# Performance work log

Measured on AMD Instinct MI355X. Metric: run time of the kernel, lower is better.

Reference implementation:

```python
import jax, jax.numpy as jnp
import numpy as np

B, S, D = 4, 4096, 128

def setup_inputs() -> dict:
    key = jax.random.key(0)
    kx, kq, kk, kv = jax.random.split(key, 4)
    x = jax.random.normal(kx, (B, S, D), dtype=jnp.float32)
    Wq = jax.random.normal(kq, (D, D), dtype=jnp.float32) * (1.0 / np.sqrt(D))
    Wk = jax.random.normal(kk, (D, D), dtype=jnp.float32) * (1.0 / np.sqrt(D))
    Wv = jax.random.normal(kv, (D, D), dtype=jnp.float32) * (1.0 / np.sqrt(D))
    return {"x": x, "Wq": Wq, "Wk": Wk, "Wv": Wv}

def reference(x, Wq, Wk, Wv):
    b, s, d = x.shape
    # nn.Linear(bias=False): y = x @ W.T
    q = jnp.einsum('bsd,ed->bse', x, Wq)
    k = jnp.einsum('bsd,ed->bse', x, Wk)
    v = jnp.einsum('bsd,ed->bse', x, Wv)
    scores = jnp.einsum('bqd,bkd->bqk', q, k) / jnp.sqrt(jnp.float32(d))
    causal = jnp.tril(jnp.ones((s, s), dtype=bool))  # [s,s]
    scores = jnp.where(causal, scores, jnp.float32(-jnp.inf))
    weights = jax.nn.softmax(scores.astype(jnp.float32), axis=-1)
    out = jnp.einsum('bqk,bkd->bqd', weights, v)
    return out  # dropout is identity in eval / p=0
```

## Files before the change

kernel.cpp:

```cpp
#include <hip/hip_runtime.h>
#include <hip/hip_bf16.h>
#include <math.h>

typedef __attribute__((ext_vector_type(8))) short short8;
typedef __attribute__((ext_vector_type(4))) float f32x4;
typedef __attribute__((ext_vector_type(4))) float float4v;
typedef __attribute__((ext_vector_type(4))) unsigned short ushort4v;

typedef __attribute__((address_space(1))) const unsigned int GAS;
typedef __attribute__((address_space(3))) unsigned int LAS;

#define B_ 4
#define S_ 4096
#define D_ 128

#define CHUNKS_PER_BATCH 288
#define NSLOT (B_ * CHUNKS_PER_BATCH)

#define LDS_K 0
#define LDS_V 16384
#define LDS_P 49152
#define LDS_TOTAL 57344

__device__ __forceinline__ unsigned short f2bf(float f) {
    union { float f; unsigned u; } v; v.f = f;
    unsigned r = v.u + 0x7FFFu + ((v.u >> 16) & 1u);
    return (unsigned short)(r >> 16);
}
__device__ __forceinline__ float bf2f(unsigned short h) {
    union { unsigned u; float f; } v; v.u = ((unsigned)h) << 16;
    return v.f;
}

__global__ void wconv_kernel(const float* __restrict__ Wq,
                             const float* __restrict__ Wk,
                             const float* __restrict__ Wv,
                             unsigned short* __restrict__ Wb) {
    int i = blockIdx.x * 256 + threadIdx.x;
    if (i >= 3 * 16384) return;
    const float* s = (i < 16384) ? Wq : (i < 32768 ? Wk : Wv);
    Wb[i] = f2bf(s[i & 16383]);
}

__global__ __launch_bounds__(256) void qkv_kernel(const float* __restrict__ X,
                                                  const unsigned short* __restrict__ Wb,
                                                  unsigned short* __restrict__ Qb,
                                                  unsigned short* __restrict__ Kb,
                                                  unsigned short* __restrict__ Vt) {
    const int tid = threadIdx.x;
    const int lane = tid & 63, w = tid >> 6;
    const int l16 = lane & 15, g = lane >> 4;
    const int r0 = blockIdx.x * 64;
    const int grp = blockIdx.y;

    const int row = r0 + w * 16 + l16;
    const float* xr = X + (long)row * 128;
    float4v x0[4], x1[4];
    #pragma unroll
    for (int kb = 0; kb < 4; ++kb) {
        x0[kb] = *reinterpret_cast<const float4v*>(xr + kb * 32 + g * 8);
        x1[kb] = *reinterpret_cast<const float4v*>(xr + kb * 32 + g * 8 + 4);
    }
    short8 a[4];
    #pragma unroll
    for (int kb = 0; kb < 4; ++kb) {
        short8 t;
        t[0] = f2bf(x0[kb][0]); t[1] = f2bf(x0[kb][1]);
        t[2] = f2bf(x0[kb][2]); t[3] = f2bf(x0[kb][3]);
        t[4] = f2bf(x1[kb][0]); t[5] = f2bf(x1[kb][1]);
        t[6] = f2bf(x1[kb][2]); t[7] = f2bf(x1[kb][3]);
        a[kb] = t;
    }

    #pragma unroll
    for (int ct = 0; ct < 8; ++ct) {
        const int e = ct * 16 + l16;
        const int c = grp * 128 + e;
        f32x4 acc = {0.f, 0.f, 0.f, 0.f};
        #pragma unroll
        for (int kb = 0; kb < 4; ++kb) {
            short8 bf = *reinterpret_cast<const short8*>(Wb + (long)c * 128 + kb * 32 + g * 8);
            acc = __builtin_amdgcn_mfma_f32_16x16x32_bf16(a[kb], bf, acc, 0, 0, 0);
        }
        const int row0 = r0 + w * 16 + g * 4;
        if (grp == 0) {
            #pragma unroll
            for (int r = 0; r < 4; ++r) Qb[(long)(row0 + r) * 128 + e] = f2bf(acc[r]);
        } else if (grp == 1) {
            #pragma unroll
            for (int r = 0; r < 4; ++r) Kb[(long)(row0 + r) * 128 + e] = f2bf(acc[r]);
        } else {
            const int bb = row0 >> 12, ss = row0 & 4095;
            ushort4v p;
            p[0] = f2bf(acc[0]); p[1] = f2bf(acc[1]); p[2] = f2bf(acc[2]); p[3] = f2bf(acc[3]);
            *reinterpret_cast<ushort4v*>(&Vt[((long)bb * 128 + e) * 4096 + ss]) = p;
        }
    }
}

__global__ __launch_bounds__(256) void attn_kernel(const unsigned short* __restrict__ Qb,
                                                   const unsigned short* __restrict__ Kb,
                                                   const unsigned short* __restrict__ Vt,
                                                   unsigned short* __restrict__ Opart,
                                                   float* __restrict__ Mpart,
                                                   float* __restrict__ Lpart) {
    __shared__ __align__(16) unsigned char lds[LDS_TOTAL];

    const int tid = threadIdx.x;
    const int lane = tid & 63, w = tid >> 6;
    const int l16 = lane & 15, g = lane >> 4;

    const int bidx = (int)blockIdx.x;
    const int b = bidx / CHUNKS_PER_BATCH;
    const int rr = bidx - b * CHUNKS_PER_BATCH;
    int gg = 0;
    while (4 * (gg + 1) * (gg + 2) <= rr) ++gg;
    const int j = rr - 4 * gg * (gg + 1);
    const int qt = 8 * gg + j / (gg + 1);
    const int c = j % (gg + 1);
    const int slot = bidx;

    const unsigned short* Qbase = Qb + (long)b * S_ * D_;
    const unsigned char* Kb_b = (const unsigned char*)(Kb + (long)b * S_ * D_);
    const unsigned char* Vb_b = (const unsigned char*)(Vt + (long)b * D_ * S_);

    const int qrow_f = qt * 64 + w * 16 + l16;
    short8 qf[4];
    #pragma unroll
    for (int kb = 0; kb < 4; ++kb)
        qf[kb] = *reinterpret_cast<const short8*>(Qbase + (long)qrow_f * 128 + kb * 32 + g * 8);

    int koff[4], voff[4];
    #pragma unroll
    for (int i = 0; i < 4; ++i) {
        int ch = w * 4 + i;
        int krow = ch * 4 + g;
        koff[i] = krow * 256 + ((l16 * 16) ^ ((krow & 7) << 4));
        int vrow = ch * 8 + (lane >> 3);
        voff[i] = vrow * 8192 + (((lane & 7) * 16) ^ ((vrow & 7) << 4));
    }

    f32x4 o[8];
    #pragma unroll
    for (int dt = 0; dt < 8; ++dt) o[dt] = (f32x4){0.f, 0.f, 0.f, 0.f};
    float m[4], lsum[4];
    int myrow[4];
    #pragma unroll
    for (int r = 0; r < 4; ++r) {
        m[r] = -INFINITY; lsum[r] = 0.f;
        myrow[r] = qt * 64 + w * 16 + g * 4 + r;
    }

    const float scale = 0.08838834764831845f;
    const int kt0 = c * 8;
    const int ktend = min(kt0 + 7, qt);

    #pragma unroll
    for (int i = 0; i < 4; ++i) {
        int ch = w * 4 + i;
        __builtin_amdgcn_global_load_lds((GAS*)(Kb_b + (long)kt0 * 16384 + koff[i]),
                                         (LAS*)(lds + LDS_K + ch * 1024), 16, 0, 0);
        __builtin_amdgcn_global_load_lds((GAS*)(Vb_b + (long)kt0 * 128 + voff[i]),
                                         (LAS*)(lds + LDS_V + (kt0 & 1) * 16384 + ch * 1024), 16, 0, 0);
    }
    __syncthreads();

    for (int kt = kt0; kt <= ktend; ++kt) {
        const int buf = kt & 1;
        const bool more = (kt < ktend);

        f32x4 s[4];
        #pragma unroll
        for (int ct = 0; ct < 4; ++ct) {
            s[ct] = (f32x4){0.f, 0.f, 0.f, 0.f};
            const int kvl = ct * 16 + l16;
            #pragma unroll
            for (int kb = 0; kb < 4; ++kb) {
                int byt = (kvl * 256 + kb * 64 + g * 16) ^ ((kvl & 7) << 4);
                short8 kf = *reinterpret_cast<const short8*>(lds + byt);
                s[ct] = __builtin_amdgcn_mfma_f32_16x16x32_bf16(qf[kb], kf, s[ct], 0, 0, 0);
            }
        }

        __syncthreads();

        if (more) {
            #pragma unroll
            for (int i = 0; i < 4; ++i) {
                int ch = w * 4 + i;
                __builtin_amdgcn_global_load_lds((GAS*)(Kb_b + (long)(kt + 1) * 16384 + koff[i]),
                                                 (LAS*)(lds + LDS_K + ch * 1024), 16, 0, 0);
                __builtin_amdgcn_global_load_lds((GAS*)(Vb_b + (long)(kt + 1) * 128 + voff[i]),
                                                 (LAS*)(lds + LDS_V + (buf ^ 1) * 16384 + ch * 1024), 16, 0, 0);
            }
        }

        const bool diag = (kt == qt);
        float rmax[4] = {-1e30f, -1e30f, -1e30f, -1e30f};
        #pragma unroll
        for (int ct = 0; ct < 4; ++ct) {
            #pragma unroll
            for (int r = 0; r < 4; ++r) {
                float sv = s[ct][r] * scale;
                if (diag && (kt * 64 + ct * 16 + l16 > myrow[r])) sv = -1e30f;
                s[ct][r] = sv;
                rmax[r] = fmaxf(rmax[r], sv);
            }
        }
        #pragma unroll
        for (int off = 1; off < 16; off <<= 1) {
            #pragma unroll
            for (int r = 0; r < 4; ++r) rmax[r] = fmaxf(rmax[r], __shfl_xor(rmax[r], off, 64));
        }
        float al[4], rsum[4];
        #pragma unroll
        for (int r = 0; r < 4; ++r) {
            float mn = fmaxf(m[r], rmax[r]);
            al[r] = __expf(m[r] - mn);
            m[r] = mn;
            rsum[r] = 0.f;
        }
        #pragma unroll
        for (int ct = 0; ct < 4; ++ct) {
            #pragma unroll
            for (int r = 0; r < 4; ++r) {
                float p = __expf(s[ct][r] - m[r]);
                s[ct][r] = p;
                rsum[r] += p;
            }
        }
        #pragma unroll
        for (int off = 1; off < 16; off <<= 1) {
            #pragma unroll
            for (int r = 0; r < 4; ++r) rsum[r] += __shfl_xor(rsum[r], off, 64);
        }
        #pragma unroll
        for (int r = 0; r < 4; ++r) lsum[r] = lsum[r] * al[r] + rsum[r];
        #pragma unroll
        for (int dt = 0; dt < 8; ++dt) {
            #pragma unroll
            for (int r = 0; r < 4; ++r) o[dt][r] *= al[r];
        }

        unsigned char* Pw = lds + LDS_P + w * 2048;
        #pragma unroll
        for (int ct = 0; ct < 4; ++ct) {
            #pragma unroll
            for (int r = 0; r < 4; ++r) {
                int pr = g * 4 + r, pc = ct * 16 + l16;
                int byt = (pr * 128 + pc * 2) ^ ((pr & 7) << 4);
                *reinterpret_cast<unsigned short*>(Pw + byt) = f2bf(s[ct][r]);
            }
        }

        #pragma unroll
        for (int kvb = 0; kvb < 2; ++kvb) {
            int pbyt = (l16 * 128 + kvb * 64 + g * 16) ^ ((l16 & 7) << 4);
            short8 pf = *reinterpret_cast<const short8*>(Pw + pbyt);
            #pragma unroll
            for (int dt = 0; dt < 8; ++dt) {
                int d = dt * 16 + l16;
                int vbyt = LDS_V + buf * 16384 + ((d * 128 + kvb * 64 + g * 16) ^ ((d & 7) << 4));
                short8 vf = *reinterpret_cast<const short8*>(lds + vbyt);
                o[dt] = __builtin_amdgcn_mfma_f32_16x16x32_bf16(pf, vf, o[dt], 0, 0, 0);
            }
        }

        if (more) __syncthreads();
    }

    unsigned short* Op = Opart + (long)slot * 8192;
    #pragma unroll
    for (int dt = 0; dt < 8; ++dt) {
        #pragma unroll
        for (int r = 0; r < 4; ++r) {
            Op[(w * 16 + g * 4 + r) * 128 + dt * 16 + l16] = f2bf(o[dt][r]);
        }
    }
    if (l16 == 0) {
        #pragma unroll
        for (int r = 0; r < 4; ++r) {
            Mpart[(long)slot * 64 + w * 16 + g * 4 + r] = m[r];
            Lpart[(long)slot * 64 + w * 16 + g * 4 + r] = lsum[r];
        }
    }
}

__global__ __launch_bounds__(256) void combine_kernel(const unsigned short* __restrict__ Opart,
                                                      const float* __restrict__ Mpart,
                                                      const float* __restrict__ Lpart,
                                                      float* __restrict__ out) {
    __shared__ float coeff[8][16];
    __shared__ float invL[16];

    const int qt = blockIdx.x >> 2, qq = blockIdx.x & 3, b = blockIdx.y;
    const int gg = qt >> 3;
    const int nc = gg + 1;
    const int slot0 = b * CHUNKS_PER_BATCH + 4 * gg * (gg + 1) + (qt - 8 * gg) * nc;
    const int r0 = qq * 16;

    const int tid = threadIdx.x;
    if (tid < 16) {
        float mg = -INFINITY;
        for (int c = 0; c < nc; ++c)
            mg = fmaxf(mg, Mpart[(long)(slot0 + c) * 64 + r0 + tid]);
        float L = 0.f;
        for (int c = 0; c < nc; ++c) {
            float co = __expf(Mpart[(long)(slot0 + c) * 64 + r0 + tid] - mg);
            coeff[c][tid] = co;
            L += co * Lpart[(long)(slot0 + c) * 64 + r0 + tid];
        }
        invL[tid] = 1.f / L;
    }
    __syncthreads();

    const int e0 = tid * 8;
    const int r = e0 >> 7;
    float acc[8];
    #pragma unroll
    for (int k = 0; k < 8; ++k) acc[k] = 0.f;
    for (int c = 0; c < nc; ++c) {
        short8 v = *reinterpret_cast<const short8*>(Opart + (long)(slot0 + c) * 8192 + r0 * 128 + e0);
        const float co = coeff[c][r];
        #pragma unroll
        for (int k = 0; k < 8; ++k)
            acc[k] += co * bf2f((unsigned short)v[k]);
    }
    const float s = invL[r];
    float4v o0, o1;
    o0[0] = acc[0] * s; o0[1] = acc[1] * s; o0[2] = acc[2] * s; o0[3] = acc[3] * s;
    o1[0] = acc[4] * s; o1[1] = acc[5] * s; o1[2] = acc[6] * s; o1[3] = acc[7] * s;
    float* dst = out + ((long)b * S_ + qt * 64 + r0) * 128 + e0;
    *reinterpret_cast<float4v*>(dst) = o0;
    *reinterpret_cast<float4v*>(dst + 4) = o1;
}

extern "C" void kernel_launch(void* const* d_in, const int* in_sizes, int n_in,
                              void* d_out, int out_size, void* d_ws, size_t ws_size,
                              hipStream_t stream) {
    (void)in_sizes; (void)n_in; (void)out_size; (void)ws_size;
    const float* x  = (const float*)d_in[0];
    const float* Wq = (const float*)d_in[1];
    const float* Wk = (const float*)d_in[2];
    const float* Wv = (const float*)d_in[3];
    float* out = (float*)d_out;

    char* ws = (char*)d_ws;
    const size_t MB4 = (size_t)16384 * 128 * 2;
    unsigned short* Qb = (unsigned short*)(ws);
    unsigned short* Kb = (unsigned short*)(ws + MB4);
    unsigned short* Vt = (unsigned short*)(ws + 2 * MB4);
    unsigned short* Wb = (unsigned short*)(ws + 3 * MB4);
    unsigned short* Opart = (unsigned short*)(ws + 3 * MB4 + (1 << 20));
    float* Mpart = (float*)(ws + 3 * MB4 + (1 << 20) + (size_t)NSLOT * 8192 * 2);
    float* Lpart = Mpart + (size_t)NSLOT * 64;

    wconv_kernel<<<192, 256, 0, stream>>>(Wq, Wk, Wv, Wb);
    qkv_kernel<<<dim3(256, 3), 256, 0, stream>>>(x, Wb, Qb, Kb, Vt);
    attn_kernel<<<NSLOT, 256, 0, stream>>>(Qb, Kb, Vt, Opart, Mpart, Lpart);
    combine_kernel<<<dim3(256, 4), 256, 0, stream>>>(Opart, Mpart, Lpart, out);
}
```

Baseline: 152.9 us.

## Load K/V fragments directly from global memory and remap blocks per XCD

Removes the LDS staging of K and V tiles (global_load_lds double buffering plus block barriers). Each wave now reads its MFMA operands straight from global memory and relies on L2 for reuse, keeping only a small LDS buffer for P. Block indices are remapped so each XCD handles one batch half, which should improve L2 locality. s_setprio is raised around the MFMA loops. The risk is that each of the 4 waves re-fetches the same K/V from cache and loses prefetch overlap, which could raise load latency.

After: 267.9 us. 75.2% more time.

```diff
diff --git a/kernel.cpp b/kernel.cpp
--- a/kernel.cpp
+++ b/kernel.cpp
@@ -7,20 +7,12 @@
 typedef __attribute__((ext_vector_type(4))) float float4v;
 typedef __attribute__((ext_vector_type(4))) unsigned short ushort4v;
 
-typedef __attribute__((address_space(1))) const unsigned int GAS;
-typedef __attribute__((address_space(3))) unsigned int LAS;
-
 #define B_ 4
 #define S_ 4096
 #define D_ 128
 
 #define CHUNKS_PER_BATCH 288
 #define NSLOT (B_ * CHUNKS_PER_BATCH)
-
-#define LDS_K 0
-#define LDS_V 16384
-#define LDS_P 49152
-#define LDS_TOTAL 57344
 
 __device__ __forceinline__ unsigned short f2bf(float f) {
     union { float f; unsigned u; } v; v.f = f;
@@ -104,41 +96,32 @@
                                                    unsigned short* __restrict__ Opart,
                                                    float* __restrict__ Mpart,
                                                    float* __restrict__ Lpart) {
-    __shared__ __align__(16) unsigned char lds[LDS_TOTAL];
+    __shared__ __align__(16) unsigned char Plds[8192];
 
     const int tid = threadIdx.x;
     const int lane = tid & 63, w = tid >> 6;
     const int l16 = lane & 15, g = lane >> 4;
 
     const int bidx = (int)blockIdx.x;
-    const int b = bidx / CHUNKS_PER_BATCH;
-    const int rr = bidx - b * CHUNKS_PER_BATCH;
+    const int xcd = bidx & 7;
+    const int b = xcd >> 1;
+    const int rr = (bidx >> 3) + (xcd & 1) * 144;
     int gg = 0;
     while (4 * (gg + 1) * (gg + 2) <= rr) ++gg;
     const int j = rr - 4 * gg * (gg + 1);
     const int qt = 8 * gg + j / (gg + 1);
     const int c = j % (gg + 1);
-    const int slot = bidx;
+    const int slot = b * CHUNKS_PER_BATCH + rr;
 
     const unsigned short* Qbase = Qb + (long)b * S_ * D_;
-    const unsigned char* Kb_b = (const unsigned char*)(Kb + (long)b * S_ * D_);
-    const unsigned char* Vb_b = (const unsigned char*)(Vt + (long)b * D_ * S_);
+    const unsigned short* Kbase = Kb + (long)b * S_ * D_;
+    const unsigned short* Vbase = Vt + (long)b * D_ * S_;
 
     const int qrow_f = qt * 64 + w * 16 + l16;
     short8 qf[4];
     #pragma unroll
     for (int kb = 0; kb < 4; ++kb)
         qf[kb] = *reinterpret_cast<const short8*>(Qbase + (long)qrow_f * 128 + kb * 32 + g * 8);
-
-    int koff[4], voff[4];
-    #pragma unroll
-    for (int i = 0; i < 4; ++i) {
-        int ch = w * 4 + i;
-        int krow = ch * 4 + g;
-        koff[i] = krow * 256 + ((l16 * 16) ^ ((krow & 7) << 4));
-        int vrow = ch * 8 + (lane >> 3);
-        voff[i] = vrow * 8192 + (((lane & 7) * 16) ^ ((vrow & 7) << 4));
-    }
 
     f32x4 o[8];
     #pragma unroll
@@ -155,45 +138,30 @@
     const int kt0 = c * 8;
     const int ktend = min(kt0 + 7, qt);
 
-    #pragma unroll
-    for (int i = 0; i < 4; ++i) {
-        int ch = w * 4 + i;
-        __builtin_amdgcn_global_load_lds((GAS*)(Kb_b + (long)kt0 * 16384 + koff[i]),
-                                         (LAS*)(lds + LDS_K + ch * 1024), 16, 0, 0);
-        __builtin_amdgcn_global_load_lds((GAS*)(Vb_b + (long)kt0 * 128 + voff[i]),
-                                         (LAS*)(lds + LDS_V + (kt0 & 1) * 16384 + ch * 1024), 16, 0, 0);
-    }
-    __syncthreads();
+    const unsigned short* kptr[4];
+    #pragma unroll
+    for (int ct = 0; ct < 4; ++ct)
+        kptr[ct] = Kbase + (long)(kt0 * 64 + ct * 16 + l16) * 128 + g * 8;
+    const unsigned short* vptr[8];
+    #pragma unroll
+    for (int dt = 0; dt < 8; ++dt)
+        vptr[dt] = Vbase + (long)(dt * 16 + l16) * 4096 + kt0 * 64 + g * 8;
+
+    unsigned char* Pw = Plds + w * 2048;
 
     for (int kt = kt0; kt <= ktend; ++kt) {
-        const int buf = kt & 1;
-        const bool more = (kt < ktend);
-
         f32x4 s[4];
+        __builtin_amdgcn_s_setprio(1);
         #pragma unroll
         for (int ct = 0; ct < 4; ++ct) {
             s[ct] = (f32x4){0.f, 0.f, 0.f, 0.f};
-            const int kvl = ct * 16 + l16;
             #pragma unroll
             for (int kb = 0; kb < 4; ++kb) {
-                int byt = (kvl * 256 + kb * 64 + g * 16) ^ ((kvl & 7) << 4);
-                short8 kf = *reinterpret_cast<const short8*>(lds + byt);
+                short8 kf = *reinterpret_cast<const short8*>(kptr[ct] + kb * 32);
                 s[ct] = __builtin_amdgcn_mfma_f32_16x16x32_bf16(qf[kb], kf, s[ct], 0, 0, 0);
             }
         }
-
-        __syncthreads();
-
-        if (more) {
-            #pragma unroll
-            for (int i = 0; i < 4; ++i) {
-                int ch = w * 4 + i;
-                __builtin_amdgcn_global_load_lds((GAS*)(Kb_b + (long)(kt + 1) * 16384 + koff[i]),
-                                                 (LAS*)(lds + LDS_K + ch * 1024), 16, 0, 0);
-                __builtin_amdgcn_global_load_lds((GAS*)(Vb_b + (long)(kt + 1) * 128 + voff[i]),
-                                                 (LAS*)(lds + LDS_V + (buf ^ 1) * 16384 + ch * 1024), 16, 0, 0);
-            }
-        }
+        __builtin_amdgcn_s_setprio(0);
 
         const bool diag = (kt == qt);
         float rmax[4] = {-1e30f, -1e30f, -1e30f, -1e30f};
@@ -242,7 +210,6 @@
             for (int r = 0; r < 4; ++r) o[dt][r] *= al[r];
         }
 
-        unsigned char* Pw = lds + LDS_P + w * 2048;
         #pragma unroll
         for (int ct = 0; ct < 4; ++ct) {
             #pragma unroll
@@ -257,16 +224,19 @@
         for (int kvb = 0; kvb < 2; ++kvb) {
             int pbyt = (l16 * 128 + kvb * 64 + g * 16) ^ ((l16 & 7) << 4);
             short8 pf = *reinterpret_cast<const short8*>(Pw + pbyt);
+            __builtin_amdgcn_s_setprio(1);
             #pragma unroll
             for (int dt = 0; dt < 8; ++dt) {
-                int d = dt * 16 + l16;
-                int vbyt = LDS_V + buf * 16384 + ((d * 128 + kvb * 64 + g * 16) ^ ((d & 7) << 4));
-                short8 vf = *reinterpret_cast<const short8*>(lds + vbyt);
+                short8 vf = *reinterpret_cast<const short8*>(vptr[dt] + kvb * 32);
                 o[dt] = __builtin_amdgcn_mfma_f32_16x16x32_bf16(pf, vf, o[dt], 0, 0, 0);
             }
-        }
-
-        if (more) __syncthreads();
+            __builtin_amdgcn_s_setprio(0);
+        }
+
+        #pragma unroll
+        for (int ct = 0; ct < 4; ++ct) kptr[ct] += 64 * 128;
+        #pragma unroll
+        for (int dt = 0; dt < 8; ++dt) vptr[dt] += 64;
     }
 
     unsigned short* Op = Opart + (long)slot * 8192;
```

## Halve KV chunk size, reverse block order, drop prefetch, lazy rescale

Applied to the files above, without the earlier changes.

Splits each query tile's KV range into chunks of 4 tiles instead of 8, which nearly doubles the number of partial-result blocks and shortens the longest block. Blocks are now launched heaviest-first. The double-buffered V prefetch is removed in favour of a synchronous load each iteration, which cuts LDS use and may raise occupancy but exposes load latency. It also adds s_setprio around the MFMA sections and skips the rescale of O and l unless the running max grows by more than 8. The combine kernel now merges more partials per row.

After: 154.8 us. No clear change (+1.3%).

```diff
diff --git a/kernel.cpp b/kernel.cpp
--- a/kernel.cpp
+++ b/kernel.cpp
@@ -14,13 +14,13 @@
 #define S_ 4096
 #define D_ 128
 
-#define CHUNKS_PER_BATCH 288
-#define NSLOT (B_ * CHUNKS_PER_BATCH)
+#define CPB 544
+#define NSLOT (B_ * CPB)
 
 #define LDS_K 0
 #define LDS_V 16384
-#define LDS_P 49152
-#define LDS_TOTAL 57344
+#define LDS_P 32768
+#define LDS_TOTAL 40960
 
 __device__ __forceinline__ unsigned short f2bf(float f) {
     union { float f; unsigned u; } v; v.f = f;
@@ -111,14 +111,14 @@
     const int l16 = lane & 15, g = lane >> 4;
 
     const int bidx = (int)blockIdx.x;
-    const int b = bidx / CHUNKS_PER_BATCH;
-    const int rr = bidx - b * CHUNKS_PER_BATCH;
+    const int b = bidx / CPB;
+    const int rr = CPB - 1 - (bidx - b * CPB);
     int gg = 0;
-    while (4 * (gg + 1) * (gg + 2) <= rr) ++gg;
-    const int j = rr - 4 * gg * (gg + 1);
-    const int qt = 8 * gg + j / (gg + 1);
+    while (2 * (gg + 1) * (gg + 2) <= rr) ++gg;
+    const int j = rr - 2 * gg * (gg + 1);
+    const int qt = 4 * gg + j / (gg + 1);
     const int c = j % (gg + 1);
-    const int slot = bidx;
+    const int slot = b * CPB + rr;
 
     const unsigned short* Qbase = Qb + (long)b * S_ * D_;
     const unsigned char* Kb_b = (const unsigned char*)(Kb + (long)b * S_ * D_);
@@ -152,24 +152,24 @@
     }
 
     const float scale = 0.08838834764831845f;
-    const int kt0 = c * 8;
-    const int ktend = min(kt0 + 7, qt);
-
-    #pragma unroll
-    for (int i = 0; i < 4; ++i) {
-        int ch = w * 4 + i;
-        __builtin_amdgcn_global_load_lds((GAS*)(Kb_b + (long)kt0 * 16384 + koff[i]),
-                                         (LAS*)(lds + LDS_K + ch * 1024), 16, 0, 0);
-        __builtin_amdgcn_global_load_lds((GAS*)(Vb_b + (long)kt0 * 128 + voff[i]),
-                                         (LAS*)(lds + LDS_V + (kt0 & 1) * 16384 + ch * 1024), 16, 0, 0);
-    }
-    __syncthreads();
+    const int kt0 = c * 4;
+    const int ktend = min(kt0 + 3, qt);
+
+    unsigned char* Pw = lds + LDS_P + w * 2048;
 
     for (int kt = kt0; kt <= ktend; ++kt) {
-        const int buf = kt & 1;
-        const bool more = (kt < ktend);
+        #pragma unroll
+        for (int i = 0; i < 4; ++i) {
+            int ch = w * 4 + i;
+            __builtin_amdgcn_global_load_lds((GAS*)(Kb_b + (long)kt * 16384 + koff[i]),
+                                             (LAS*)(lds + LDS_K + ch * 1024), 16, 0, 0);
+            __builtin_amdgcn_global_load_lds((GAS*)(Vb_b + (long)kt * 128 + voff[i]),
+                                             (LAS*)(lds + LDS_V + ch * 1024), 16, 0, 0);
+        }
+        __syncthreads();
 
         f32x4 s[4];
+        __builtin_amdgcn_s_setprio(1);
         #pragma unroll
         for (int ct = 0; ct < 4; ++ct) {
             s[ct] = (f32x4){0.f, 0.f, 0.f, 0.f};
@@ -181,19 +181,7 @@
                 s[ct] = __builtin_amdgcn_mfma_f32_16x16x32_bf16(qf[kb], kf, s[ct], 0, 0, 0);
             }
         }
-
-        __syncthreads();
-
-        if (more) {
-            #pragma unroll
-            for (int i = 0; i < 4; ++i) {
-                int ch = w * 4 + i;
-                __builtin_amdgcn_global_load_lds((GAS*)(Kb_b + (long)(kt + 1) * 16384 + koff[i]),
-                                                 (LAS*)(lds + LDS_K + ch * 1024), 16, 0, 0);
-                __builtin_amdgcn_global_load_lds((GAS*)(Vb_b + (long)(kt + 1) * 128 + voff[i]),
-                                                 (LAS*)(lds + LDS_V + (buf ^ 1) * 16384 + ch * 1024), 16, 0, 0);
-            }
-        }
+        __builtin_amdgcn_s_setprio(0);
 
         const bool diag = (kt == qt);
         float rmax[4] = {-1e30f, -1e30f, -1e30f, -1e30f};
@@ -212,14 +200,25 @@
             #pragma unroll
             for (int r = 0; r < 4; ++r) rmax[r] = fmaxf(rmax[r], __shfl_xor(rmax[r], off, 64));
         }
-        float al[4], rsum[4];
-        #pragma unroll
-        for (int r = 0; r < 4; ++r) {
-            float mn = fmaxf(m[r], rmax[r]);
-            al[r] = __expf(m[r] - mn);
-            m[r] = mn;
-            rsum[r] = 0.f;
-        }
+        bool upd = false;
+        #pragma unroll
+        for (int r = 0; r < 4; ++r) upd = upd || (rmax[r] > m[r] + 8.0f);
+        if (__any(upd)) {
+            float al[4];
+            #pragma unroll
+            for (int r = 0; r < 4; ++r) {
+                float mn = fmaxf(m[r], rmax[r]);
+                al[r] = __expf(m[r] - mn);
+                m[r] = mn;
+                lsum[r] *= al[r];
+            }
+            #pragma unroll
+            for (int dt = 0; dt < 8; ++dt) {
+                #pragma unroll
+                for (int r = 0; r < 4; ++r) o[dt][r] *= al[r];
+            }
+        }
+        float rsum[4] = {0.f, 0.f, 0.f, 0.f};
         #pragma unroll
         for (int ct = 0; ct < 4; ++ct) {
             #pragma unroll
@@ -235,14 +234,8 @@
             for (int r = 0; r < 4; ++r) rsum[r] += __shfl_xor(rsum[r], off, 64);
         }
         #pragma unroll
-        for (int r = 0; r < 4; ++r) lsum[r] = lsum[r] * al[r] + rsum[r];
-        #pragma unroll
-        for (int dt = 0; dt < 8; ++dt) {
-            #pragma unroll
-            for (int r = 0; r < 4; ++r) o[dt][r] *= al[r];
-        }
-
-        unsigned char* Pw = lds + LDS_P + w * 2048;
+        for (int r = 0; r < 4; ++r) lsum[r] += rsum[r];
+
         #pragma unroll
         for (int ct = 0; ct < 4; ++ct) {
             #pragma unroll
@@ -257,16 +250,18 @@
         for (int kvb = 0; kvb < 2; ++kvb) {
             int pbyt = (l16 * 128 + kvb * 64 + g * 16) ^ ((l16 & 7) << 4);
             short8 pf = *reinterpret_cast<const short8*>(Pw + pbyt);
+            __builtin_amdgcn_s_setprio(1);
             #pragma unroll
             for (int dt = 0; dt < 8; ++dt) {
                 int d = dt * 16 + l16;
-                int vbyt = LDS_V + buf * 16384 + ((d * 128 + kvb * 64 + g * 16) ^ ((d & 7) << 4));
+                int vbyt = LDS_V + ((d * 128 + kvb * 64 + g * 16) ^ ((d & 7) << 4));
                 short8 vf = *reinterpret_cast<const short8*>(lds + vbyt);
                 o[dt] = __builtin_amdgcn_mfma_f32_16x16x32_bf16(pf, vf, o[dt], 0, 0, 0);
             }
-        }
-
-        if (more) __syncthreads();
+            __builtin_amdgcn_s_setprio(0);
+        }
+
+        if (kt < ktend) __syncthreads();
     }
 
     unsigned short* Op = Opart + (long)slot * 8192;
@@ -290,13 +285,13 @@
                                                       const float* __restrict__ Mpart,
                                                       const float* __restrict__ Lpart,
                                                       float* __restrict__ out) {
-    __shared__ float coeff[8][16];
+    __shared__ float coeff[16][16];
     __shared__ float invL[16];
 
     const int qt = blockIdx.x >> 2, qq = blockIdx.x & 3, b = blockIdx.y;
-    const int gg = qt >> 3;
+    const int gg = qt >> 2;
     const int nc = gg + 1;
-    const int slot0 = b * CHUNKS_PER_BATCH + 4 * gg * (gg + 1) + (qt - 8 * gg) * nc;
+    const int slot0 = b * CPB + 2 * gg * (gg + 1) + (qt - 4 * gg) * nc;
     const int r0 = qq * 16;
 
     const int tid = threadIdx.x;
```
